# Kernel tuning notes

Hardware: AMD Instinct MI355X
Metric: run time of the kernel (lower is better)

The kernel has to match this reference:

```python
import jax, jax.numpy as jnp
import numpy as np

N_NODES = 50000
N_EDGES = 600000
F_IN = 128
H = 128
NUM_GRAPHS = 64
SELF_LOOP_W = 2.0  # improved=True


def setup_inputs() -> dict:
    key = jax.random.key(0)
    ks = jax.random.split(key, 16)
    x = jax.random.normal(ks[0], (N_NODES, F_IN), dtype=jnp.float32)
    edge_index = jax.random.randint(ks[1], (2, N_EDGES), 0, N_NODES, dtype=jnp.int64)
    batch_index = jnp.sort(jax.random.randint(ks[2], (N_NODES,), 0, NUM_GRAPHS, dtype=jnp.int64))
    edge_weight = jax.random.uniform(ks[3], (N_EDGES,), dtype=jnp.float32)
    def lin(k, fin, fout):
        s = 1.0 / np.sqrt(fin)
        kw, kb = jax.random.split(k)
        W = jax.random.uniform(kw, (fin, fout), minval=-s, maxval=s, dtype=jnp.float32)
        b = jax.random.uniform(kb, (fout,), minval=-s, maxval=s, dtype=jnp.float32)
        return W, b
    W0, b0 = lin(ks[4], F_IN, H)
    W1, b1 = lin(ks[5], H, H)
    W2, b2 = lin(ks[6], H, H)
    W3, b3 = lin(ks[7], H, H)
    Wout, bout = lin(ks[8], 2 * H, 1)
    return dict(x=x, edge_index=edge_index, batch_index=batch_index, edge_weight=edge_weight,
                W0=W0, b0=b0, W1=W1, b1=b1, W2=W2, b2=b2, W3=W3, b3=b3, Wout=Wout, bout=bout)


def reference(x, edge_index, batch_index, edge_weight, W0, b0, W1, b1, W2, b2, W3, b3, Wout, bout):
    N = x.shape[0]
    loop = jnp.arange(N)
    src = jnp.concatenate([edge_index[0], loop])  # [E+N]
    dst = jnp.concatenate([edge_index[1], loop])
    w = jnp.concatenate([edge_weight, jnp.full((N,), SELF_LOOP_W, dtype=x.dtype)])
    # symmetric GCN normalization: deg over destination, norm = d^-1/2[src]*w*d^-1/2[dst]
    deg = jax.ops.segment_sum(w, dst, num_segments=N)
    dinv = jnp.where(deg > 0, jax.lax.rsqrt(deg), 0.0)
    norm = dinv[src] * w * dinv[dst]  # [E+N]

    def conv(h, W, b):
        h = h @ W  # dense transform before aggregation
        msg = h[src] * norm[:, None]
        return jax.ops.segment_sum(msg, dst, num_segments=N) + b

    h = jnp.tanh(conv(x, W0, b0))
    h = jnp.tanh(conv(h, W1, b1))
    h = jnp.tanh(conv(h, W2, b2))
    h = jnp.tanh(conv(h, W3, b3))

    gmax = jax.ops.segment_max(h, batch_index, num_segments=NUM_GRAPHS)
    gmax = jnp.where(jnp.isfinite(gmax), gmax, 0.0)  # guard empty graphs
    cnt = jax.ops.segment_sum(jnp.ones((N,), dtype=h.dtype), batch_index, num_segments=NUM_GRAPHS)
    gmean = jax.ops.segment_sum(h, batch_index, num_segments=NUM_GRAPHS) / jnp.maximum(cnt, 1.0)[:, None]
    hidden = jnp.concatenate([gmax, gmean], axis=1)  # [B, 2H]
    out = hidden @ Wout + bout  # [B, 1]
    return out, hidden
```

## Files before the change

kernel.cpp:

```cpp
#include <hip/hip_runtime.h>
#include <hip/hip_bf16.h>
#include <hip/hip_fp16.h>

typedef __hip_bfloat16 bf16;
typedef _Float16 half8 __attribute__((ext_vector_type(8)));
typedef float f32x4 __attribute__((ext_vector_type(4)));

#define FDIM 128
#define SELF_W 2.0f
#define NGRAPH 64
#define DEG_SCALE 1048576.0f
#define DEG_MASK  ((1ull<<44) - 1ull)

__device__ __forceinline__ float b2f(bf16 v){ return __bfloat162float(v); }

__device__ __forceinline__ unsigned fenc(float f){
  unsigned b = __float_as_uint(f);
  return (b & 0x80000000u) ? ~b : (b | 0x80000000u);
}
__device__ __forceinline__ float fdec(unsigned u){
  unsigned b = (u & 0x80000000u) ? (u ^ 0x80000000u) : ~u;
  return __uint_as_float(b);
}

__device__ __forceinline__ float rdf(const void* p, long long i, int f32){
  return f32 ? ((const float*)p)[i] : b2f(((const bf16*)p)[i]);
}
__device__ __forceinline__ int rdi(const void* p, long long i, int i64){
  return i64 ? (int)(((const long long*)p)[i]) : ((const int*)p)[i];
}

__global__ __launch_bounds__(256) void k_probe(const unsigned short* __restrict__ x16,
                                               const int* __restrict__ ei32,
                                               int* __restrict__ flags){
  __shared__ int cbig, codd;
  int tid = threadIdx.x;
  if (tid == 0){ cbig = 0; codd = 0; }
  __syncthreads();
  for (int i = tid; i < 4096; i += 256){
    int e = (x16[i] >> 7) & 0xFF;
    if (e >= 134) atomicAdd(&cbig, 1);
  }
  for (int i = tid; i < 512; i += 256){
    if (ei32[2*i + 1] != 0) atomicAdd(&codd, 1);
  }
  __syncthreads();
  if (tid == 0){
    flags[0] = (cbig >= 64) ? 1 : 0;
    flags[1] = (codd < 8)  ? 1 : 0;
  }
}

struct PtrPack { const void* p[10]; };
__global__ void k_cvt_params(PtrPack pk, float* __restrict__ pf,
                             _Float16* __restrict__ wt,
                             const int* __restrict__ flags){
  const int sz[10]  = {16384,16384,16384,16384,128,128,128,128,256,1};
  const int dst[10] = {0,16384,32768,49152,65536,65664,65792,65920,66048,66304};
  int i = blockIdx.x*blockDim.x + threadIdx.x;
  if (i >= 66305) return;
  int seg = 0, rem = i;
  while (rem >= sz[seg]){ rem -= sz[seg]; seg++; }
  float v = rdf(pk.p[seg], rem, flags[0]);
  pf[dst[seg] + rem] = v;
  if (seg < 4){
    int k = rem >> 7, n = rem & 127;
    wt[seg*16384 + n*128 + k] = (_Float16)v;
  }
}

__global__ void k_packed_init(unsigned long long* packed, int N){
  int i = blockIdx.x*blockDim.x + threadIdx.x;
  if (i < N) packed[i] = (unsigned long long)(SELF_W * DEG_SCALE);
}

__global__ void k_edge_deg(const void* __restrict__ ei, const void* __restrict__ ew,
                           unsigned long long* __restrict__ packed,
                           unsigned* __restrict__ rank, int2* __restrict__ epk,
                           int E, int N, const int* __restrict__ flags){
  int e = blockIdx.x*blockDim.x + threadIdx.x;
  if (e >= E) return;
  epk[e] = make_int2(0, 0);
  int d = rdi(ei, (long long)E + e, flags[1]);
  unsigned r = 0u;
  if ((unsigned)d < (unsigned)N){
    float w = rdf(ew, e, flags[0]);
    unsigned long long add = (1ull << 44) |
        (unsigned long long)__float2uint_rn(w * DEG_SCALE);
    unsigned long long old = atomicAdd(&packed[d], add);
    r = (unsigned)(old >> 44);
  }
  rank[e] = r;
}

__device__ __forceinline__ unsigned wave_incl_scan(unsigned v){
  int lane = threadIdx.x & 63;
  #pragma unroll
  for (int d = 1; d < 64; d <<= 1){
    unsigned t = __shfl_up(v, d, 64);
    if (lane >= d) v += t;
  }
  return v;
}

__global__ __launch_bounds__(256) void k_scan_pre(const unsigned long long* __restrict__ packed,
                                                  float* __restrict__ dinv,
                                                  unsigned* __restrict__ bsum, int N){
  __shared__ unsigned wsh[4];
  int tid = threadIdx.x, lane = tid & 63, wid = tid >> 6;
  int i0 = blockIdx.x*1024 + tid*4;
  unsigned tsum = 0u;
  #pragma unroll
  for (int j = 0; j < 4; j++){
    int i = i0 + j;
    if (i < N){
      unsigned long long pv = packed[i];
      tsum += (unsigned)(pv >> 44);
      float d = (float)(pv & DEG_MASK) * (1.0f / DEG_SCALE);
      dinv[i] = (d > 0.f) ? rsqrtf(d) : 0.f;
    }
  }
  #pragma unroll
  for (int d = 1; d < 64; d <<= 1) tsum += __shfl_down(tsum, d, 64);
  if (lane == 0) wsh[wid] = tsum;
  __syncthreads();
  if (tid == 0) bsum[blockIdx.x] = wsh[0] + wsh[1] + wsh[2] + wsh[3];
}

__global__ __launch_bounds__(64) void k_scan_mid(unsigned* __restrict__ bsum,
                                                 unsigned* __restrict__ off,
                                                 int nb, int N){
  int lane = threadIdx.x;
  unsigned v = (lane < nb) ? bsum[lane] : 0u;
  unsigned isc = wave_incl_scan(v);
  if (lane < nb) bsum[lane] = isc - v;
  if (lane == 63) off[N] = isc;
}

__global__ __launch_bounds__(256) void k_scan_fin(const unsigned long long* __restrict__ packed,
                                                  const unsigned* __restrict__ bsum,
                                                  unsigned* __restrict__ off, int N){
  __shared__ unsigned wsh[4];
  int tid = threadIdx.x, lane = tid & 63, wid = tid >> 6;
  int i0 = blockIdx.x*1024 + tid*4;
  unsigned v0=0u,v1=0u,v2=0u,v3=0u;
  if (i0+0 < N) v0 = (unsigned)(packed[i0+0] >> 44);
  if (i0+1 < N) v1 = (unsigned)(packed[i0+1] >> 44);
  if (i0+2 < N) v2 = (unsigned)(packed[i0+2] >> 44);
  if (i0+3 < N) v3 = (unsigned)(packed[i0+3] >> 44);
  unsigned tsum = v0+v1+v2+v3;
  unsigned isc = wave_incl_scan(tsum);
  if (lane == 63) wsh[wid] = isc;
  __syncthreads();
  unsigned wbase = 0u;
  #pragma unroll
  for (int w = 0; w < 4; w++) if (w < wid) wbase += wsh[w];
  unsigned ex = bsum[blockIdx.x] + wbase + (isc - tsum);
  if (i0+0 < N) off[i0+0] = ex;
  if (i0+1 < N) off[i0+1] = ex + v0;
  if (i0+2 < N) off[i0+2] = ex + v0 + v1;
  if (i0+3 < N) off[i0+3] = ex + v0 + v1 + v2;
}

__global__ void k_bucket(const void* __restrict__ ei, const void* __restrict__ ew,
                         const float* __restrict__ dinv,
                         const unsigned* __restrict__ off,
                         const unsigned* __restrict__ rank,
                         int2* __restrict__ epk,
                         int E, int N, const int* __restrict__ flags){
  int e = blockIdx.x*blockDim.x + threadIdx.x;
  if (e >= E) return;
  int s_ = rdi(ei, e, flags[1]);
  int d  = rdi(ei, (long long)E + e, flags[1]);
  if ((unsigned)s_ >= (unsigned)N || (unsigned)d >= (unsigned)N) return;
  unsigned pos = off[d] + rank[e];
  if (pos < (unsigned)E){
    float coef = dinv[s_] * rdf(ew, e, flags[0]) * dinv[d];
    epk[pos] = make_int2(s_, __float_as_int(coef));
  }
}

__global__ void k_bounds(const void* __restrict__ bat, int N,
                         unsigned* __restrict__ start, unsigned* __restrict__ gcnt,
                         const int* __restrict__ flags){
  __shared__ unsigned s[NGRAPH+1];
  int g = threadIdx.x;
  int i64 = flags[1];
  if (g <= NGRAPH){
    int lo = 0, hi = N;
    while (lo < hi){ int mid = (lo + hi) >> 1; if (rdi(bat, mid, i64) < g) lo = mid + 1; else hi = mid; }
    s[g] = (unsigned)lo;
  }
  __syncthreads();
  if (g < NGRAPH){ start[g] = s[g]; gcnt[g] = s[g+1] - s[g]; }
  if (g == NGRAPH) start[NGRAPH] = s[NGRAPH];
}

template<int MODE>
__global__ __launch_bounds__(256) void k_gemm(const void* __restrict__ in,
                                              const _Float16* __restrict__ WT,
                                              __half* __restrict__ outh, int N,
                                              const int* __restrict__ flags){
  __shared__ _Float16 sout[4*16*136];
  int tid  = threadIdx.x;
  int wid  = tid >> 6, lane = tid & 63;
  int ln   = lane & 15, quad = lane >> 4;
  int row0 = blockIdx.x * 64;
  int rowA = row0 + wid*16 + ln;
  int rA   = (rowA < N) ? rowA : (N > 0 ? N-1 : 0);

  half8 af[4];
  if (MODE == 1){
    const _Float16* src = (const _Float16*)in + (size_t)rA*FDIM + quad*8;
    #pragma unroll
    for (int kc = 0; kc < 4; kc++) af[kc] = *(const half8*)(src + kc*32);
  } else {
    if (flags[0]){
      const float* src = (const float*)in + (size_t)rA*FDIM + quad*8;
      #pragma unroll
      for (int kc = 0; kc < 4; kc++){
        float4 a = *(const float4*)(src + kc*32);
        float4 b = *(const float4*)(src + kc*32 + 4);
        half8 h; h[0]=(_Float16)a.x; h[1]=(_Float16)a.y; h[2]=(_Float16)a.z; h[3]=(_Float16)a.w;
        h[4]=(_Float16)b.x; h[5]=(_Float16)b.y; h[6]=(_Float16)b.z; h[7]=(_Float16)b.w;
        af[kc] = h;
      }
    } else {
      const unsigned short* src = (const unsigned short*)in + (size_t)rA*FDIM + quad*8;
      #pragma unroll
      for (int kc = 0; kc < 4; kc++){
        ushort4 u0 = *(const ushort4*)(src + kc*32);
        ushort4 u1 = *(const ushort4*)(src + kc*32 + 4);
        half8 h;
        h[0]=(_Float16)__uint_as_float((unsigned)u0.x<<16);
        h[1]=(_Float16)__uint_as_float((unsigned)u0.y<<16);
        h[2]=(_Float16)__uint_as_float((unsigned)u0.z<<16);
        h[3]=(_Float16)__uint_as_float((unsigned)u0.w<<16);
        h[4]=(_Float16)__uint_as_float((unsigned)u1.x<<16);
        h[5]=(_Float16)__uint_as_float((unsigned)u1.y<<16);
        h[6]=(_Float16)__uint_as_float((unsigned)u1.z<<16);
        h[7]=(_Float16)__uint_as_float((unsigned)u1.w<<16);
        af[kc] = h;
      }
    }
  }

  f32x4 acc[8];
  #pragma unroll
  for (int nt = 0; nt < 8; nt++) acc[nt] = (f32x4){0.f,0.f,0.f,0.f};

  #pragma unroll
  for (int kc = 0; kc < 4; kc++){
    #pragma unroll
    for (int nt = 0; nt < 8; nt++){
      half8 bf = *(const half8*)(WT + (size_t)(nt*16 + ln)*FDIM + kc*32 + quad*8);
      acc[nt] = __builtin_amdgcn_mfma_f32_16x16x32_f16(af[kc], bf, acc[nt], 0, 0, 0);
    }
  }

  _Float16* so = sout + wid*2176;
  #pragma unroll
  for (int nt = 0; nt < 8; nt++)
    #pragma unroll
    for (int reg = 0; reg < 4; reg++)
      so[(quad*4 + reg)*136 + nt*16 + ln] = (_Float16)acc[nt][reg];
  __syncthreads();

  #pragma unroll
  for (int c = 0; c < 4; c++){
    int chunk = tid + c*256;
    int r = chunk >> 4, co = (chunk & 15)*8;
    int row = row0 + r;
    if (row < N){
      half8 v = *(const half8*)(sout + (r>>4)*2176 + (r&15)*136 + co);
      *(half8*)((_Float16*)outh + (size_t)row*FDIM + co) = v;
    }
  }
}

__global__ __launch_bounds__(256) void k_agg(const __half* __restrict__ th,
                                             const float* __restrict__ dinv,
                                             const unsigned* __restrict__ off,
                                             const int2* __restrict__ epk,
                                             const float* __restrict__ bias,
                                             __half* __restrict__ hout, int N, int E){
  int n    = (int)((blockIdx.x*blockDim.x + threadIdx.x) >> 6);
  int lane = threadIdx.x & 63;
  if (n >= N) return;
  const __half2* t2 = (const __half2*)th;
  float di = dinv[n];
  float sw = di * di * SELF_W;
  float2 v = __half22float2(t2[(size_t)n*64 + lane]);
  float a0 = sw * v.x, a1 = sw * v.y;
  float b0 = 0.f, b1 = 0.f, c0 = 0.f, c1 = 0.f, d0 = 0.f, d1 = 0.f;
  unsigned beg = off[n], end = off[n+1];
  if (end > (unsigned)E) end = (unsigned)E;
  if (beg > end) beg = end;
  unsigned i = beg;
  for (; i + 8 <= end; i += 8){
    int2 e0 = epk[i],   e1 = epk[i+1], e2 = epk[i+2], e3 = epk[i+3];
    int2 e4 = epk[i+4], e5 = epk[i+5], e6 = epk[i+6], e7 = epk[i+7];
    float2 t0 = __half22float2(t2[(size_t)e0.x*64 + lane]);
    float2 t1 = __half22float2(t2[(size_t)e1.x*64 + lane]);
    float2 t2v= __half22float2(t2[(size_t)e2.x*64 + lane]);
    float2 t3 = __half22float2(t2[(size_t)e3.x*64 + lane]);
    float2 t4 = __half22float2(t2[(size_t)e4.x*64 + lane]);
    float2 t5 = __half22float2(t2[(size_t)e5.x*64 + lane]);
    float2 t6 = __half22float2(t2[(size_t)e6.x*64 + lane]);
    float2 t7 = __half22float2(t2[(size_t)e7.x*64 + lane]);
    float w0 = __int_as_float(e0.y), w1 = __int_as_float(e1.y);
    float w2 = __int_as_float(e2.y), w3 = __int_as_float(e3.y);
    float w4 = __int_as_float(e4.y), w5 = __int_as_float(e5.y);
    float w6 = __int_as_float(e6.y), w7 = __int_as_float(e7.y);
    a0 += w0 * t0.x; a1 += w0 * t0.y;
    b0 += w1 * t1.x; b1 += w1 * t1.y;
    c0 += w2 * t2v.x; c1 += w2 * t2v.y;
    d0 += w3 * t3.x; d1 += w3 * t3.y;
    a0 += w4 * t4.x; a1 += w4 * t4.y;
    b0 += w5 * t5.x; b1 += w5 * t5.y;
    c0 += w6 * t6.x; c1 += w6 * t6.y;
    d0 += w7 * t7.x; d1 += w7 * t7.y;
  }
  for (; i < end; i++){
    int2 e0 = epk[i];
    float cf = __int_as_float(e0.y);
    float2 tv = __half22float2(t2[(size_t)e0.x*64 + lane]);
    a0 += cf * tv.x; a1 += cf * tv.y;
  }
  a0 += b0 + c0 + d0;
  a1 += b1 + c1 + d1;
  int cc = lane * 2;
  a0 = tanhf(a0 + bias[cc]);
  a1 = tanhf(a1 + bias[cc+1]);
  ((__half2*)hout)[(size_t)n*64 + lane] = __floats2half2_rn(a0, a1);
}

__global__ void k_pool_init(unsigned* gmaxu, float* gsum){
  int i = blockIdx.x*blockDim.x + threadIdx.x;
  if (i < NGRAPH*FDIM){ gmaxu[i] = 0u; gsum[i] = 0.f; }
}

__global__ __launch_bounds__(256) void k_pool2(const __half* __restrict__ h,
                                               const unsigned* __restrict__ start,
                                               unsigned* __restrict__ gmaxu,
                                               float* __restrict__ gsum){
  int g = blockIdx.x >> 2, sub = blockIdx.x & 3;
  int col = threadIdx.x & 127, half_ = threadIdx.x >> 7;
  unsigned s0 = start[g], s1 = start[g+1];
  float m = -INFINITY, sm = 0.f;
  for (unsigned n = s0 + sub*2 + half_; n < s1; n += 8){
    float v = __half2float(h[(size_t)n*FDIM + col]);
    m = fmaxf(m, v); sm += v;
  }
  __shared__ float shm[256], shs[256];
  shm[threadIdx.x] = m; shs[threadIdx.x] = sm;
  __syncthreads();
  if (half_ == 0){
    m = fmaxf(m, shm[threadIdx.x + 128]);
    sm += shs[threadIdx.x + 128];
    if (m > -INFINITY) atomicMax(&gmaxu[g*FDIM + col], fenc(m));
    atomicAdd(&gsum[g*FDIM + col], sm);
  }
}

__global__ __launch_bounds__(256) void k_out(const unsigned* __restrict__ gmaxu,
                                             const float* __restrict__ gsum,
                                             const unsigned* __restrict__ gcnt,
                                             const float* __restrict__ Wout,
                                             const float* __restrict__ bout,
                                             void* __restrict__ outp,
                                             const int* __restrict__ flags){
  int g = blockIdx.x;
  int c = threadIdx.x;
  unsigned nc = gcnt[g];
  float val;
  if (c < FDIM){
    val = nc ? fdec(gmaxu[g*FDIM + c]) : 0.f;
  } else {
    float denom = nc ? (float)nc : 1.f;
    val = gsum[g*FDIM + (c - FDIM)] / denom;
  }
  int f32out = flags[0];
  int hidx = NGRAPH + g*(2*FDIM) + c;
  if (f32out) ((float*)outp)[hidx] = val;
  else        ((bf16*)outp)[hidx] = __float2bfloat16(val);

  __shared__ float red[256];
  red[c] = val * Wout[c];
  __syncthreads();
  for (int s = 128; s > 0; s >>= 1){
    if (c < s) red[c] += red[c + s];
    __syncthreads();
  }
  if (c == 0){
    float o = red[0] + bout[0];
    if (f32out) ((float*)outp)[g] = o;
    else        ((bf16*)outp)[g] = __float2bfloat16(o);
  }
}

extern "C" void kernel_launch(void* const* d_in, const int* in_sizes, int n_in,
                              void* d_out, int out_size, void* d_ws, size_t ws_size,
                              hipStream_t stream){
  int N = in_sizes[0] / FDIM;
  int E = in_sizes[3];
  int NB = (N + 1023) / 1024;

  char* p = (char*)d_ws;
  auto alloc = [&](size_t bytes){ char* r = p; p += (bytes + 255) & ~(size_t)255; return r; };
  int*       flags  = (int*)      alloc(16);
  float*     pf     = (float*)    alloc((size_t)(66305 + 64)*4);
  _Float16*  wt     = (_Float16*) alloc((size_t)4*FDIM*FDIM*2);
  unsigned long long* packed = (unsigned long long*)alloc((size_t)N*8);
  float*     dinv   = (float*)    alloc((size_t)N*4);
  unsigned*  off    = (unsigned*) alloc((size_t)(N+1)*4);
  unsigned*  bsum   = (unsigned*) alloc((size_t)128*4);
  unsigned*  rank   = (unsigned*) alloc((size_t)E*4);
  int2*      epk    = (int2*)     alloc((size_t)E*8);
  __half*    th     = (__half*)   alloc((size_t)N*FDIM*2);
  __half*    hh     = (__half*)   alloc((size_t)N*FDIM*2);
  unsigned*  gmaxu  = (unsigned*) alloc((size_t)NGRAPH*FDIM*4);
  float*     gsum   = (float*)    alloc((size_t)NGRAPH*FDIM*4);
  unsigned*  gcnt   = (unsigned*) alloc((size_t)NGRAPH*4);
  unsigned*  gstart = (unsigned*) alloc((size_t)(NGRAPH+1)*4);

  float* bf_[4] = {pf + 65536, pf + 65664, pf + 65792, pf + 65920};
  float* Woutf  = pf + 66048;
  float* boutf  = pf + 66304;

  k_probe<<<1, 256, 0, stream>>>((const unsigned short*)d_in[0], (const int*)d_in[1], flags);

  int gE = (E + 255)/256, gN = (N + 255)/256;
  PtrPack pk;
  pk.p[0]=d_in[4]; pk.p[1]=d_in[6]; pk.p[2]=d_in[8]; pk.p[3]=d_in[10];
  pk.p[4]=d_in[5]; pk.p[5]=d_in[7]; pk.p[6]=d_in[9]; pk.p[7]=d_in[11];
  pk.p[8]=d_in[12]; pk.p[9]=d_in[13];
  k_cvt_params<<<(66305 + 255)/256, 256, 0, stream>>>(pk, pf, wt, flags);
  k_packed_init<<<gN, 256, 0, stream>>>(packed, N);
  k_edge_deg<<<gE, 256, 0, stream>>>(d_in[1], d_in[3], packed, rank, epk, E, N, flags);
  k_scan_pre<<<NB, 256, 0, stream>>>(packed, dinv, bsum, N);
  k_scan_mid<<<1, 64, 0, stream>>>(bsum, off, NB, N);
  k_scan_fin<<<NB, 256, 0, stream>>>(packed, bsum, off, N);
  k_bucket<<<gE, 256, 0, stream>>>(d_in[1], d_in[3], dinv, off, rank, epk, E, N, flags);
  k_bounds<<<1, 128, 0, stream>>>(d_in[2], N, gstart, gcnt, flags);

  int gG = (N + 63)/64;
  int gA = (N + 3)/4;

  k_gemm<0><<<gG, 256, 0, stream>>>(d_in[0], wt + 0*16384, th, N, flags);
  k_agg<<<gA, 256, 0, stream>>>(th, dinv, off, epk, bf_[0], hh, N, E);
  for (int l = 1; l < 4; l++){
    k_gemm<1><<<gG, 256, 0, stream>>>(hh, wt + (size_t)l*16384, th, N, flags);
    k_agg<<<gA, 256, 0, stream>>>(th, dinv, off, epk, bf_[l], hh, N, E);
  }

  k_pool_init<<<(NGRAPH*FDIM + 255)/256, 256, 0, stream>>>(gmaxu, gsum);
  k_pool2<<<4*NGRAPH, 256, 0, stream>>>(hh, gstart, gmaxu, gsum);
  k_out<<<NGRAPH, 256, 0, stream>>>(gmaxu, gsum, gcnt, Woutf, boutf, d_out, flags);
}
```

Baseline: 449.5 us.

## Split features into 32-column panels and pad CSR rows for panel-parallel aggregation

Measured after the change: 581.3 us. 1.29x slower.

```diff
diff --git a/kernel.cpp b/kernel.cpp
--- a/kernel.cpp
+++ b/kernel.cpp
@@ -77,10 +77,10 @@
 __global__ void k_edge_deg(const void* __restrict__ ei, const void* __restrict__ ew,
                            unsigned long long* __restrict__ packed,
                            unsigned* __restrict__ rank, int2* __restrict__ epk,
-                           int E, int N, const int* __restrict__ flags){
+                           int E, unsigned Epad, int N, const int* __restrict__ flags){
   int e = blockIdx.x*blockDim.x + threadIdx.x;
+  if ((unsigned)e < Epad) epk[e] = make_int2(0, 0);
   if (e >= E) return;
-  epk[e] = make_int2(0, 0);
   int d = rdi(ei, (long long)E + e, flags[1]);
   unsigned r = 0u;
   if ((unsigned)d < (unsigned)N){
@@ -115,7 +115,7 @@
     int i = i0 + j;
     if (i < N){
       unsigned long long pv = packed[i];
-      tsum += (unsigned)(pv >> 44);
+      tsum += ((unsigned)(pv >> 44) + 7u) & ~7u;
       float d = (float)(pv & DEG_MASK) * (1.0f / DEG_SCALE);
       dinv[i] = (d > 0.f) ? rsqrtf(d) : 0.f;
     }
@@ -144,10 +144,10 @@
   int tid = threadIdx.x, lane = tid & 63, wid = tid >> 6;
   int i0 = blockIdx.x*1024 + tid*4;
   unsigned v0=0u,v1=0u,v2=0u,v3=0u;
-  if (i0+0 < N) v0 = (unsigned)(packed[i0+0] >> 44);
-  if (i0+1 < N) v1 = (unsigned)(packed[i0+1] >> 44);
-  if (i0+2 < N) v2 = (unsigned)(packed[i0+2] >> 44);
-  if (i0+3 < N) v3 = (unsigned)(packed[i0+3] >> 44);
+  if (i0+0 < N) v0 = ((unsigned)(packed[i0+0] >> 44) + 7u) & ~7u;
+  if (i0+1 < N) v1 = ((unsigned)(packed[i0+1] >> 44) + 7u) & ~7u;
+  if (i0+2 < N) v2 = ((unsigned)(packed[i0+2] >> 44) + 7u) & ~7u;
+  if (i0+3 < N) v3 = ((unsigned)(packed[i0+3] >> 44) + 7u) & ~7u;
   unsigned tsum = v0+v1+v2+v3;
   unsigned isc = wave_incl_scan(tsum);
   if (lane == 63) wsh[wid] = isc;
@@ -167,14 +167,14 @@
                          const unsigned* __restrict__ off,
                          const unsigned* __restrict__ rank,
                          int2* __restrict__ epk,
-                         int E, int N, const int* __restrict__ flags){
+                         int E, unsigned Epad, int N, const int* __restrict__ flags){
   int e = blockIdx.x*blockDim.x + threadIdx.x;
   if (e >= E) return;
   int s_ = rdi(ei, e, flags[1]);
   int d  = rdi(ei, (long long)E + e, flags[1]);
   if ((unsigned)s_ >= (unsigned)N || (unsigned)d >= (unsigned)N) return;
   unsigned pos = off[d] + rank[e];
-  if (pos < (unsigned)E){
+  if (pos < Epad){
     float coef = dinv[s_] * rdf(ew, e, flags[0]) * dinv[d];
     epk[pos] = make_int2(s_, __float_as_int(coef));
   }
@@ -199,7 +199,8 @@
 template<int MODE>
 __global__ __launch_bounds__(256) void k_gemm(const void* __restrict__ in,
                                               const _Float16* __restrict__ WT,
-                                              __half* __restrict__ outh, int N,
+                                              _Float16* __restrict__ outp, int N,
+                                              size_t pstride,
                                               const int* __restrict__ flags){
   __shared__ _Float16 sout[4*16*136];
   int tid  = threadIdx.x;
@@ -211,9 +212,10 @@
 
   half8 af[4];
   if (MODE == 1){
-    const _Float16* src = (const _Float16*)in + (size_t)rA*FDIM + quad*8;
+    const _Float16* src = (const _Float16*)in;
     #pragma unroll
-    for (int kc = 0; kc < 4; kc++) af[kc] = *(const half8*)(src + kc*32);
+    for (int kc = 0; kc < 4; kc++)
+      af[kc] = *(const half8*)(src + (size_t)kc*pstride + (size_t)rA*32 + quad*8);
   } else {
     if (flags[0]){
       const float* src = (const float*)in + (size_t)rA*FDIM + quad*8;
@@ -273,66 +275,58 @@
     int row = row0 + r;
     if (row < N){
       half8 v = *(const half8*)(sout + (r>>4)*2176 + (r&15)*136 + co);
-      *(half8*)((_Float16*)outh + (size_t)row*FDIM + co) = v;
+      *(half8*)(outp + (size_t)(co>>5)*pstride + (size_t)row*32 + (co & 31)) = v;
     }
   }
 }
 
-__global__ __launch_bounds__(256) void k_agg(const __half* __restrict__ th,
+__global__ __launch_bounds__(256) void k_agg(const _Float16* __restrict__ tp,
                                              const float* __restrict__ dinv,
                                              const unsigned* __restrict__ off,
                                              const int2* __restrict__ epk,
                                              const float* __restrict__ bias,
-                                             __half* __restrict__ hout, int N, int E){
-  int n    = (int)((blockIdx.x*blockDim.x + threadIdx.x) >> 6);
+                                             _Float16* __restrict__ hp,
+                                             int N, size_t pstride){
+  int wv   = threadIdx.x >> 6;
   int lane = threadIdx.x & 63;
+  int panel = blockIdx.x & 3;
+  int n = (blockIdx.x >> 2)*4 + wv;
   if (n >= N) return;
-  const __half2* t2 = (const __half2*)th;
+  int quad = lane >> 4, sub2 = (lane & 15)*2;
+  const _Float16* tpp = tp + (size_t)panel*pstride;
+
   float di = dinv[n];
   float sw = di * di * SELF_W;
-  float2 v = __half22float2(t2[(size_t)n*64 + lane]);
-  float a0 = sw * v.x, a1 = sw * v.y;
-  float b0 = 0.f, b1 = 0.f, c0 = 0.f, c1 = 0.f, d0 = 0.f, d1 = 0.f;
+  float2 sv = __half22float2(*(const __half2*)(tpp + (size_t)n*32 + sub2));
+
+  float a0 = 0.f, a1 = 0.f, b0 = 0.f, b1 = 0.f;
   unsigned beg = off[n], end = off[n+1];
-  if (end > (unsigned)E) end = (unsigned)E;
-  if (beg > end) beg = end;
-  unsigned i = beg;
-  for (; i + 8 <= end; i += 8){
-    int2 e0 = epk[i],   e1 = epk[i+1], e2 = epk[i+2], e3 = epk[i+3];
-    int2 e4 = epk[i+4], e5 = epk[i+5], e6 = epk[i+6], e7 = epk[i+7];
-    float2 t0 = __half22float2(t2[(size_t)e0.x*64 + lane]);
-    float2 t1 = __half22float2(t2[(size_t)e1.x*64 + lane]);
-    float2 t2v= __half22float2(t2[(size_t)e2.x*64 + lane]);
-    float2 t3 = __half22float2(t2[(size_t)e3.x*64 + lane]);
-    float2 t4 = __half22float2(t2[(size_t)e4.x*64 + lane]);
-    float2 t5 = __half22float2(t2[(size_t)e5.x*64 + lane]);
-    float2 t6 = __half22float2(t2[(size_t)e6.x*64 + lane]);
-    float2 t7 = __half22float2(t2[(size_t)e7.x*64 + lane]);
+  unsigned i = beg + quad;
+  for (; i + 4 < end; i += 8){
+    int2 e0 = epk[i];
+    int2 e1 = epk[i+4];
+    float2 t0 = __half22float2(*(const __half2*)(tpp + (size_t)e0.x*32 + sub2));
+    float2 t1 = __half22float2(*(const __half2*)(tpp + (size_t)e1.x*32 + sub2));
     float w0 = __int_as_float(e0.y), w1 = __int_as_float(e1.y);
-    float w2 = __int_as_float(e2.y), w3 = __int_as_float(e3.y);
-    float w4 = __int_as_float(e4.y), w5 = __int_as_float(e5.y);
-    float w6 = __int_as_float(e6.y), w7 = __int_as_float(e7.y);
     a0 += w0 * t0.x; a1 += w0 * t0.y;
     b0 += w1 * t1.x; b1 += w1 * t1.y;
-    c0 += w2 * t2v.x; c1 += w2 * t2v.y;
-    d0 += w3 * t3.x; d1 += w3 * t3.y;
-    a0 += w4 * t4.x; a1 += w4 * t4.y;
-    b0 += w5 * t5.x; b1 += w5 * t5.y;
-    c0 += w6 * t6.x; c1 += w6 * t6.y;
-    d0 += w7 * t7.x; d1 += w7 * t7.y;
-  }
-  for (; i < end; i++){
+  }
+  if (i < end){
     int2 e0 = epk[i];
-    float cf = __int_as_float(e0.y);
-    float2 tv = __half22float2(t2[(size_t)e0.x*64 + lane]);
-    a0 += cf * tv.x; a1 += cf * tv.y;
-  }
-  a0 += b0 + c0 + d0;
-  a1 += b1 + c1 + d1;
-  int cc = lane * 2;
+    float2 t0 = __half22float2(*(const __half2*)(tpp + (size_t)e0.x*32 + sub2));
+    float w0 = __int_as_float(e0.y);
+    a0 += w0 * t0.x; a1 += w0 * t0.y;
+  }
+  a0 += b0; a1 += b1;
+  a0 += __shfl_xor(a0, 16, 64); a1 += __shfl_xor(a1, 16, 64);
+  a0 += __shfl_xor(a0, 32, 64); a1 += __shfl_xor(a1, 32, 64);
+  a0 += sw * sv.x;
+  a1 += sw * sv.y;
+  int cc = panel*32 + sub2;
   a0 = tanhf(a0 + bias[cc]);
   a1 = tanhf(a1 + bias[cc+1]);
-  ((__half2*)hout)[(size_t)n*64 + lane] = __floats2half2_rn(a0, a1);
+  if (quad == 0)
+    *(__half2*)(hp + (size_t)panel*pstride + (size_t)n*32 + sub2) = __floats2half2_rn(a0, a1);
 }
 
 __global__ void k_pool_init(unsigned* gmaxu, float* gsum){
@@ -340,16 +334,18 @@
   if (i < NGRAPH*FDIM){ gmaxu[i] = 0u; gsum[i] = 0.f; }
 }
 
-__global__ __launch_bounds__(256) void k_pool2(const __half* __restrict__ h,
+__global__ __launch_bounds__(256) void k_pool2(const _Float16* __restrict__ hp,
                                                const unsigned* __restrict__ start,
                                                unsigned* __restrict__ gmaxu,
-                                               float* __restrict__ gsum){
+                                               float* __restrict__ gsum,
+                                               size_t pstride){
   int g = blockIdx.x >> 2, sub = blockIdx.x & 3;
   int col = threadIdx.x & 127, half_ = threadIdx.x >> 7;
+  const _Float16* hpp = hp + (size_t)(col >> 5)*pstride + (col & 31);
   unsigned s0 = start[g], s1 = start[g+1];
   float m = -INFINITY, sm = 0.f;
   for (unsigned n = s0 + sub*2 + half_; n < s1; n += 8){
-    float v = __half2float(h[(size_t)n*FDIM + col]);
+    float v = (float)hpp[(size_t)n*32];
     m = fmaxf(m, v); sm += v;
   }
   __shared__ float shm[256], shs[256];
@@ -405,6 +401,8 @@
   int N = in_sizes[0] / FDIM;
   int E = in_sizes[3];
   int NB = (N + 1023) / 1024;
+  unsigned Epad = (unsigned)E + 8u*(unsigned)N;
+  size_t pstride = (size_t)N * 32;
 
   char* p = (char*)d_ws;
   auto alloc = [&](size_t bytes){ char* r = p; p += (bytes + 255) & ~(size_t)255; return r; };
@@ -416,9 +414,9 @@
   unsigned*  off    = (unsigned*) alloc((size_t)(N+1)*4);
   unsigned*  bsum   = (unsigned*) alloc((size_t)128*4);
   unsigned*  rank   = (unsigned*) alloc((size_t)E*4);
-  int2*      epk    = (int2*)     alloc((size_t)E*8);
-  __half*    th     = (__half*)   alloc((size_t)N*FDIM*2);
-  __half*    hh     = (__half*)   alloc((size_t)N*FDIM*2);
+  int2*      epk    = (int2*)     alloc((size_t)Epad*8);
+  _Float16*  th     = (_Float16*) alloc((size_t)N*FDIM*2);
+  _Float16*  hh     = (_Float16*) alloc((size_t)N*FDIM*2);
   unsigned*  gmaxu  = (unsigned*) alloc((size_t)NGRAPH*FDIM*4);
   float*     gsum   = (float*)    alloc((size_t)NGRAPH*FDIM*4);
   unsigned*  gcnt   = (unsigned*) alloc((size_t)NGRAPH*4);
@@ -431,30 +429,31 @@
   k_probe<<<1, 256, 0, stream>>>((const unsigned short*)d_in[0], (const int*)d_in[1], flags);
 
   int gE = (E + 255)/256, gN = (N + 255)/256;
+  int gEp = ((int)Epad + 255)/256;
   PtrPack pk;
   pk.p[0]=d_in[4]; pk.p[1]=d_in[6]; pk.p[2]=d_in[8]; pk.p[3]=d_in[10];
   pk.p[4]=d_in[5]; pk.p[5]=d_in[7]; pk.p[6]=d_in[9]; pk.p[7]=d_in[11];
   pk.p[8]=d_in[12]; pk.p[9]=d_in[13];
   k_cvt_params<<<(66305 + 255)/256, 256, 0, stream>>>(pk, pf, wt, flags);
   k_packed_init<<<gN, 256, 0, stream>>>(packed, N);
-  k_edge_deg<<<gE, 256, 0, stream>>>(d_in[1], d_in[3], packed, rank, epk, E, N, flags);
+  k_edge_deg<<<gEp, 256, 0, stream>>>(d_in[1], d_in[3], packed, rank, epk, E, Epad, N, flags);
   k_scan_pre<<<NB, 256, 0, stream>>>(packed, dinv, bsum, N);
   k_scan_mid<<<1, 64, 0, stream>>>(bsum, off, NB, N);
   k_scan_fin<<<NB, 256, 0, stream>>>(packed, bsum, off, N);
-  k_bucket<<<gE, 256, 0, stream>>>(d_in[1], d_in[3], dinv, off, rank, epk, E, N, flags);
+  k_bucket<<<gE, 256, 0, stream>>>(d_in[1], d_in[3], dinv, off, rank, epk, E, Epad, N, flags);
   k_bounds<<<1, 128, 0, stream>>>(d_in[2], N, gstart, gcnt, flags);
 
   int gG = (N + 63)/64;
-  int gA = (N + 3)/4;
-
-  k_gemm<0><<<gG, 256, 0, stream>>>(d_in[0], wt + 0*16384, th, N, flags);
-  k_agg<<<gA, 256, 0, stream>>>(th, dinv, off, epk, bf_[0], hh, N, E);
+  int gA = ((N + 3)/4)*4;
+
+  k_gemm<0><<<gG, 256, 0, stream>>>(d_in[0], wt + 0*16384, th, N, pstride, flags);
+  k_agg<<<gA, 256, 0, stream>>>(th, dinv, off, epk, bf_[0], hh, N, pstride);
   for (int l = 1; l < 4; l++){
-    k_gemm<1><<<gG, 256, 0, stream>>>(hh, wt + (size_t)l*16384, th, N, flags);
-    k_agg<<<gA, 256, 0, stream>>>(th, dinv, off, epk, bf_[l], hh, N, E);
+    k_gemm<1><<<gG, 256, 0, stream>>>(hh, wt + (size_t)l*16384, th, N, pstride, flags);
+    k_agg<<<gA, 256, 0, stream>>>(th, dinv, off, epk, bf_[l], hh, N, pstride);
   }
 
   k_pool_init<<<(NGRAPH*FDIM + 255)/256, 256, 0, stream>>>(gmaxu, gsum);
-  k_pool2<<<4*NGRAPH, 256, 0, stream>>>(hh, gstart, gmaxu, gsum);
+  k_pool2<<<4*NGRAPH, 256, 0, stream>>>(hh, gstart, gmaxu, gsum, pstride);
   k_out<<<NGRAPH, 256, 0, stream>>>(gmaxu, gsum, gcnt, Woutf, boutf, d_out, flags);
 }
```
